# Performance work log

Hardware: AMD Instinct MI355X
Metric: run time of the kernel (lower is better)

The kernel has to match this reference:

```python
import jax, jax.numpy as jnp
import numpy as np
from jax import lax

B_SZ, SEQ, D_MODEL = 4, 1024, 1024
D_STATE, D_CONV, EXPAND = 16, 4, 2
D_INNER = EXPAND * D_MODEL
EPS = 1e-6


def layernorm(x, alpha, bias):
    # torch.std default is unbiased (ddof=1)
    mean = x.mean(axis=-1, keepdims=True)
    std = jnp.sqrt(jnp.var(x, axis=-1, keepdims=True, ddof=1))
    return alpha * (x - mean) / (std + EPS) + bias


def setup_inputs() -> dict:
    key = jax.random.key(0)
    ks = jax.random.split(key, 8)
    std = 0.02
    A = jnp.tile(jnp.arange(1, D_STATE + 1, dtype=jnp.float32)[None, :], (D_INNER, 1))
    return {
        "x": jax.random.normal(ks[0], (B_SZ, SEQ, D_MODEL), jnp.float32),
        "in_proj_w": jax.random.normal(ks[1], (2 * D_INNER, D_MODEL), jnp.float32) * std,
        "in_proj_b": jnp.zeros((2 * D_INNER,), jnp.float32),
        "conv_w": jax.random.normal(ks[2], (D_INNER, 1, D_CONV), jnp.float32) * std,
        "conv_b": jnp.zeros((D_INNER,), jnp.float32),
        "x_proj_w": jax.random.normal(ks[3], (2 * D_STATE, D_INNER), jnp.float32) * std,
        "x_proj_b": jnp.zeros((2 * D_STATE,), jnp.float32),
        "dt_proj_w": jax.random.normal(ks[4], (D_INNER, D_INNER), jnp.float32) * std,
        "dt_proj_b": jnp.zeros((D_INNER,), jnp.float32),
        "A_log": jnp.log(A),
        "D_param": jnp.ones((D_INNER,), jnp.float32),
        "out_proj_w": jax.random.normal(ks[5], (D_MODEL, D_INNER), jnp.float32) * std,
        "out_proj_b": jnp.zeros((D_MODEL,), jnp.float32),
        "norm_alpha": jnp.ones((D_MODEL,), jnp.float32),
        "norm_bias": jnp.zeros((D_MODEL,), jnp.float32),
        "in_norm_alpha": jnp.ones((D_MODEL,), jnp.float32),
        "in_norm_bias": jnp.zeros((D_MODEL,), jnp.float32),
    }


def selective_scan(x_conv, delta, A, Bm, Cm, D_param):
    # x_conv, delta: (B, L, E); A: (E, N); Bm, Cm: (B, L, N)
    L = x_conv.shape[1]

    def step(h, inp):
        xt, dt, bt, ct, t = inp  # (B,E),(B,E),(B,N),(B,N),()
        dA = jnp.exp(jnp.clip(dt[..., None] * A, -10.0, 0.0))          # (B,E,N)
        dBx = dt[..., None] * bt[:, None, :] * xt[..., None]           # (B,E,N)
        h = dA * h + dBx
        # periodic renormalization every 16 steps
        hn = jnp.clip(jnp.linalg.norm(h, axis=-1, keepdims=True), 1e-6, None)
        scale = jnp.where(hn > 10.0, 10.0 / hn, jnp.ones_like(hn))
        h = jnp.where(t % 16 == 15, h * scale, h)
        y = jnp.einsum('bn,ben->be', ct, h) + D_param * xt
        return h, y

    h0 = jnp.zeros((x_conv.shape[0], x_conv.shape[2], A.shape[1]), x_conv.dtype)
    xs = (x_conv.swapaxes(0, 1), delta.swapaxes(0, 1),
          Bm.swapaxes(0, 1), Cm.swapaxes(0, 1), jnp.arange(L))
    _, ys = lax.scan(step, h0, xs)
    return ys.swapaxes(0, 1)  # (B, L, E)


def reference(x, in_proj_w, in_proj_b, conv_w, conv_b, x_proj_w, x_proj_b,
              dt_proj_w, dt_proj_b, A_log, D_param, out_proj_w, out_proj_b,
              norm_alpha, norm_bias, in_norm_alpha, in_norm_bias):
    residual = x
    xn = layernorm(x, in_norm_alpha, in_norm_bias)
    xz = xn @ in_proj_w.T + in_proj_b                  # (B, L, 2E)
    x_in, z = jnp.split(xz, 2, axis=-1)
    # causal depthwise conv: pad left d_conv-1, no right pad == torch pad + truncate
    xc = lax.conv_general_dilated(
        x_in.swapaxes(1, 2), conv_w, window_strides=(1,),
        padding=[(D_CONV - 1, 0)], feature_group_count=D_INNER,
        dimension_numbers=('NCH', 'OIH', 'NCH')) + conv_b[None, :, None]
    x_conv = jax.nn.silu(xc.swapaxes(1, 2))            # (B, L, E)
    bc = x_conv @ x_proj_w.T + x_proj_b                # (B, L, 2N)
    Bm, Cm = jnp.split(bc, 2, axis=-1)
    delta = jax.nn.softplus(x_conv @ dt_proj_w.T + dt_proj_b)
    delta = jnp.clip(delta, 1e-4, 10.0)
    A = -jnp.exp(A_log)
    y = selective_scan(x_conv, delta, A, Bm, Cm, D_param)
    y = y * jax.nn.silu(z)
    out = y @ out_proj_w.T + out_proj_b
    # dropout is identity in eval mode
    return layernorm(residual + out, norm_alpha, norm_bias)
```

## Files before the change

### kernel.cpp

```cpp
#include <hip/hip_runtime.h>
#include <hip/hip_bf16.h>
#include <hip/hip_fp16.h>

#define B_SZ   4
#define SEQ    1024
#define DMODEL 1024
#define DSTATE 16
#define DINNER 2048
#define NROWS  (B_SZ * SEQ)
#define NCHUNK 64
#define NCHAIN (B_SZ * DINNER)
#define NDTXP  2176

typedef __attribute__((ext_vector_type(8))) _Float16 half8;
typedef __attribute__((ext_vector_type(4))) float f32x4;

__device__ __forceinline__ void gload_lds16(const void* g, void* l) {
  __builtin_amdgcn_global_load_lds(
      (const __attribute__((address_space(1))) unsigned int*)g,
      (__attribute__((address_space(3))) unsigned int*)l, 16, 0, 0);
}

__global__ __launch_bounds__(256) void f2h_pad(const float* __restrict__ src,
                                               _Float16* __restrict__ dst,
                                               int n_src, int n_dst) {
  int i = blockIdx.x * 256 + threadIdx.x;
  if (i < n_src) dst[i] = (_Float16)src[i];
  else if (i < n_dst) dst[i] = (_Float16)0.f;
}

__global__ __launch_bounds__(256) void concat_dtxp_w(const float* __restrict__ dt_w,
                                                     const float* __restrict__ xp_w,
                                                     _Float16* __restrict__ w) {
  int i = blockIdx.x * 256 + threadIdx.x;
  if (i >= NDTXP * DINNER) return;
  int row = i >> 11;
  float v = 0.f;
  if (row < 2048) v = dt_w[i];
  else if (row < 2080) v = xp_w[i - 2048 * DINNER];
  w[i] = (_Float16)v;
}
__global__ __launch_bounds__(256) void concat_dtxp_b(const float* __restrict__ dt_b,
                                                     const float* __restrict__ xp_b,
                                                     float* __restrict__ bias) {
  int i = blockIdx.x * 256 + threadIdx.x;
  if (i >= NDTXP) return;
  float v = 0.f;
  if (i < 2048) v = dt_b[i];
  else if (i < 2080) v = xp_b[i - 2048];
  bias[i] = v;
}

__global__ __launch_bounds__(256) void ln_kernel(
    const float* __restrict__ x, const float* __restrict__ alpha,
    const float* __restrict__ beta, _Float16* __restrict__ out_h) {
  int row = blockIdx.x, tid = threadIdx.x;
  float4 v = ((const float4*)(x + (size_t)row * DMODEL))[tid];
  float s  = v.x + v.y + v.z + v.w;
  float ss = v.x * v.x + v.y * v.y + v.z * v.z + v.w * v.w;
#pragma unroll
  for (int off = 1; off < 64; off <<= 1) {
    s += __shfl_xor(s, off);
    ss += __shfl_xor(ss, off);
  }
  __shared__ float red[8];
  int wid = tid >> 6, lane = tid & 63;
  if (lane == 0) { red[wid] = s; red[4 + wid] = ss; }
  __syncthreads();
  s = red[0] + red[1] + red[2] + red[3];
  ss = red[4] + red[5] + red[6] + red[7];
  float mean = s * (1.f / DMODEL);
  float var = (ss - (float)DMODEL * mean * mean) * (1.f / (DMODEL - 1));
  float inv = 1.f / (sqrtf(fmaxf(var, 0.f)) + 1e-6f);
  float4 al = ((const float4*)alpha)[tid];
  float4 be = ((const float4*)beta)[tid];
  _Float16* o = out_h + (size_t)row * DMODEL + tid * 4;
  o[0] = (_Float16)(al.x * (v.x - mean) * inv + be.x);
  o[1] = (_Float16)(al.y * (v.y - mean) * inv + be.y);
  o[2] = (_Float16)(al.z * (v.z - mean) * inv + be.z);
  o[3] = (_Float16)(al.w * (v.w - mean) * inv + be.w);
}

__global__ __launch_bounds__(256) void ln2_kernel(
    const float* __restrict__ x, const float* __restrict__ part,
    const float* __restrict__ alpha, const float* __restrict__ beta,
    float* __restrict__ out_f) {
  int row = blockIdx.x, tid = threadIdx.x;
  float4 v = ((const float4*)(x + (size_t)row * DMODEL))[tid];
  float4 a = ((const float4*)(part + (size_t)row * DMODEL))[tid];
  float4 b = ((const float4*)(part + (size_t)NROWS * DMODEL + (size_t)row * DMODEL))[tid];
  v.x += a.x + b.x; v.y += a.y + b.y; v.z += a.z + b.z; v.w += a.w + b.w;
  float s  = v.x + v.y + v.z + v.w;
  float ss = v.x * v.x + v.y * v.y + v.z * v.z + v.w * v.w;
#pragma unroll
  for (int off = 1; off < 64; off <<= 1) {
    s += __shfl_xor(s, off);
    ss += __shfl_xor(ss, off);
  }
  __shared__ float red[8];
  int wid = tid >> 6, lane = tid & 63;
  if (lane == 0) { red[wid] = s; red[4 + wid] = ss; }
  __syncthreads();
  s = red[0] + red[1] + red[2] + red[3];
  ss = red[4] + red[5] + red[6] + red[7];
  float mean = s * (1.f / DMODEL);
  float var = (ss - (float)DMODEL * mean * mean) * (1.f / (DMODEL - 1));
  float inv = 1.f / (sqrtf(fmaxf(var, 0.f)) + 1e-6f);
  float4 al = ((const float4*)alpha)[tid];
  float4 be = ((const float4*)beta)[tid];
  float4 r;
  r.x = al.x * (v.x - mean) * inv + be.x;
  r.y = al.y * (v.y - mean) * inv + be.y;
  r.z = al.z * (v.z - mean) * inv + be.z;
  r.w = al.w * (v.w - mean) * inv + be.w;
  ((float4*)(out_f + (size_t)row * DMODEL))[tid] = r;
}

template <int EPI, int BN>
__global__ __launch_bounds__(256, 4) void gemm_bt(
    const _Float16* __restrict__ A, const _Float16* __restrict__ B,
    const float* __restrict__ bias,
    void* __restrict__ Co, void* __restrict__ Co2,
    int lda, int ldb, int K, int ldc) {
  __shared__ __align__(16) _Float16 As[128 * 64];
  __shared__ __align__(16) _Float16 Bs[BN * 64];
  constexpr int NF = BN / 32;
  const int tid = threadIdx.x;
  const int nwgx = gridDim.x;
  const int nwg = nwgx * gridDim.y;
  const int orig = blockIdx.y * nwgx + blockIdx.x;
  const int cpx = nwg >> 3;
  const int id = (orig & 7) * cpx + (orig >> 3);
  const int m0 = (id / nwgx) * 128, n0 = (id % nwgx) * BN;
  const size_t koff = (size_t)blockIdx.z * K;

  const int lane = tid & 63;
  const int wid = tid >> 6;
  const int wr = wid >> 1, wc = wid & 1;
  const int r16 = lane & 15, q = lane >> 4;

  const int srow = tid >> 3, sslot = tid & 7;

  int aoff[2][4], boff[2][NF];
#pragma unroll
  for (int kk = 0; kk < 2; ++kk) {
#pragma unroll
    for (int mi = 0; mi < 4; ++mi) {
      int r = wr * 64 + mi * 16 + r16;
      aoff[kk][mi] = r * 128 + ((((kk << 2) + q) ^ (r & 7)) << 4);
    }
#pragma unroll
    for (int ni = 0; ni < NF; ++ni) {
      int r = wc * (BN / 2) + ni * 16 + r16;
      boff[kk][ni] = r * 128 + ((((kk << 2) + q) ^ (r & 7)) << 4);
    }
  }

  f32x4 acc[4][NF] = {};
  for (int k0 = 0; k0 < K; k0 += 64) {
    __syncthreads();
#pragma unroll
    for (int p = 0; p < 4; ++p) {
      int row = p * 32 + srow;
      int gs = sslot ^ (row & 7);
      gload_lds16(A + (size_t)(m0 + row) * lda + koff + k0 + gs * 8,
                  (char*)As + (p * 256 + tid) * 16);
    }
#pragma unroll
    for (int p = 0; p < BN / 32; ++p) {
      int row = p * 32 + srow;
      int gs = sslot ^ (row & 7);
      gload_lds16(B + (size_t)(n0 + row) * ldb + koff + k0 + gs * 8,
                  (char*)Bs + (p * 256 + tid) * 16);
    }
    __syncthreads();
#pragma unroll
    for (int kk = 0; kk < 2; ++kk) {
      half8 af[4], bf[NF];
#pragma unroll
      for (int mi = 0; mi < 4; ++mi) af[mi] = *(const half8*)((const char*)As + aoff[kk][mi]);
#pragma unroll
      for (int ni = 0; ni < NF; ++ni) bf[ni] = *(const half8*)((const char*)Bs + boff[kk][ni]);
#pragma unroll
      for (int mi = 0; mi < 4; ++mi)
#pragma unroll
        for (int ni = 0; ni < NF; ++ni)
          acc[mi][ni] =
              __builtin_amdgcn_mfma_f32_16x16x32_f16(af[mi], bf[ni], acc[mi][ni], 0, 0, 0);
    }
  }

#pragma unroll
  for (int mi = 0; mi < 4; ++mi) {
    int row = m0 + wr * 64 + mi * 16 + q * 4;
#pragma unroll
    for (int ni = 0; ni < NF; ++ni) {
      int col = n0 + wc * (BN / 2) + ni * 16 + r16;
      float bs = (blockIdx.z == 0) ? bias[col] : 0.f;
#pragma unroll
      for (int rr = 0; rr < 4; ++rr) {
        float v = acc[mi][ni][rr] + bs;
        if (EPI == 0) {
          ((_Float16*)Co)[(size_t)(row + rr) * ldc + col] = (_Float16)v;
        } else if (EPI == 2) {
          ((float*)Co)[(size_t)blockIdx.z * NROWS * ldc +
                       (size_t)(row + rr) * ldc + col] = v;
        } else {
          if (col < 2048) {
            float sp = v > 15.f ? v : log1pf(__expf(v));
            ((_Float16*)Co)[(size_t)(row + rr) * 2048 + col] =
                (_Float16)fminf(10.f, fmaxf(1e-4f, sp));
          } else {
            ((float*)Co2)[(size_t)(row + rr) * 128 + (col - 2048)] = v;
          }
        }
      }
    }
  }
}

__global__ __launch_bounds__(256) void conv_silu(const _Float16* __restrict__ xz,
                                                 const float* __restrict__ w,
                                                 const float* __restrict__ cb,
                                                 _Float16* __restrict__ xc) {
  int idx = blockIdx.x * 256 + threadIdx.x;
  int e = idx & (DINNER - 1);
  int t = (idx >> 11) & (SEQ - 1);
  int b = idx >> 21;
  const _Float16* base = xz + (size_t)b * SEQ * (2 * DINNER) + e;
  float acc = cb[e];
  float4 wv = *(const float4*)(w + e * 4);
  const float* wp = (const float*)&wv;
#pragma unroll
  for (int j = 0; j < 4; ++j) {
    int tt = t - 3 + j;
    if (tt >= 0) acc += wp[j] * (float)base[(size_t)tt * (2 * DINNER)];
  }
  float r = acc / (1.f + __expf(-acc));
  xc[idx] = (_Float16)r;
}

__global__ __launch_bounds__(256) void scan_p1(
    const _Float16* __restrict__ xc, const _Float16* __restrict__ dth,
    const float* __restrict__ bcp, const float* __restrict__ A_log,
    _Float16* __restrict__ Pout, _Float16* __restrict__ Qout) {
  int tid = threadIdx.x;
  int bx = blockIdx.x;
  int c = bx >> 5;
  int b = (bx >> 3) & 3;
  int e = ((bx & 7) << 8) + tid;
  float A[16];
  {
    const float4* ap = (const float4*)(A_log + (size_t)e * DSTATE);
#pragma unroll
    for (int i = 0; i < 4; ++i) {
      float4 v = ap[i];
      A[4 * i + 0] = -__expf(v.x); A[4 * i + 1] = -__expf(v.y);
      A[4 * i + 2] = -__expf(v.z); A[4 * i + 3] = -__expf(v.w);
    }
  }
  size_t row0 = (size_t)b * SEQ + (size_t)c * 16;
  const _Float16* pdt = dth + row0 * DINNER + e;
  const _Float16* px  = xc  + row0 * DINNER + e;
  const float*    pb  = bcp + row0 * 128;
  float P[16], q[16];
#pragma unroll
  for (int n = 0; n < 16; ++n) { P[n] = 1.f; q[n] = 0.f; }
  for (int u = 0; u < 16; ++u) {
    float dtv = (float)pdt[(size_t)u * DINNER];
    float xv  = (float)px[(size_t)u * DINNER];
    float dtx = dtv * xv;
    const float4* Bp = (const float4*)(pb + (size_t)u * 128);
    float Bv[16];
#pragma unroll
    for (int i = 0; i < 4; ++i) {
      float4 t4 = Bp[i];
      Bv[4 * i + 0] = t4.x; Bv[4 * i + 1] = t4.y;
      Bv[4 * i + 2] = t4.z; Bv[4 * i + 3] = t4.w;
    }
#pragma unroll
    for (int n = 0; n < 16; ++n) {
      float da = __expf(fmaxf(dtv * A[n], -10.f));
      P[n] *= da;
      q[n] = da * q[n] + dtx * Bv[n];
    }
  }
  size_t chain = (size_t)b * DINNER + e;
  size_t base = ((size_t)c * NCHAIN + chain) * 16;
  half8 p0, p1, q0, q1;
#pragma unroll
  for (int n = 0; n < 8; ++n) {
    p0[n] = (_Float16)P[n]; p1[n] = (_Float16)P[n + 8];
    q0[n] = (_Float16)q[n]; q1[n] = (_Float16)q[n + 8];
  }
  ((half8*)(Pout + base))[0] = p0; ((half8*)(Pout + base))[1] = p1;
  ((half8*)(Qout + base))[0] = q0; ((half8*)(Qout + base))[1] = q1;
}

__global__ __launch_bounds__(256) void scan_p2(
    _Float16* __restrict__ Pbuf, const _Float16* __restrict__ Qbuf) {
  int chain = blockIdx.x * 256 + threadIdx.x;
  float h[16];
#pragma unroll
  for (int n = 0; n < 16; ++n) h[n] = 0.f;
  for (int c = 0; c < NCHUNK; ++c) {
    size_t base = ((size_t)c * NCHAIN + chain) * 16;
    half8 p0 = ((const half8*)(Pbuf + base))[0];
    half8 p1 = ((const half8*)(Pbuf + base))[1];
    half8 q0 = ((const half8*)(Qbuf + base))[0];
    half8 q1 = ((const half8*)(Qbuf + base))[1];
    float hold[16];
#pragma unroll
    for (int n = 0; n < 16; ++n) hold[n] = h[n];
#pragma unroll
    for (int n = 0; n < 8; ++n) {
      h[n]     = (float)p0[n] * h[n]     + (float)q0[n];
      h[n + 8] = (float)p1[n] * h[n + 8] + (float)q1[n];
    }
    float hn2 = 0.f;
#pragma unroll
    for (int n = 0; n < 16; ++n) hn2 += h[n] * h[n];
    float hn = fmaxf(sqrtf(hn2), 1e-6f);
    if (hn > 10.f) {
      float sc = 10.f / hn;
#pragma unroll
      for (int n = 0; n < 16; ++n) h[n] *= sc;
    }
    if (c > 0) {
      size_t pb2 = ((size_t)(c - 1) * NCHAIN + chain) * 16;
      half8 s0, s1;
#pragma unroll
      for (int n = 0; n < 8; ++n) {
        s0[n] = (_Float16)hold[n]; s1[n] = (_Float16)hold[n + 8];
      }
      ((half8*)(Pbuf + pb2))[0] = s0;
      ((half8*)(Pbuf + pb2))[1] = s1;
    }
  }
}

__global__ __launch_bounds__(256) void scan_p3(
    const _Float16* __restrict__ xc, const _Float16* __restrict__ dth,
    const float* __restrict__ bcp, const _Float16* __restrict__ xz,
    const float* __restrict__ A_log, const float* __restrict__ Dp,
    const _Float16* __restrict__ Hbuf, _Float16* __restrict__ y) {
  int tid = threadIdx.x;
  int bx = blockIdx.x;
  int c = bx >> 5;
  int b = (bx >> 3) & 3;
  int e = ((bx & 7) << 8) + tid;
  float A[16];
  {
    const float4* ap = (const float4*)(A_log + (size_t)e * DSTATE);
#pragma unroll
    for (int i = 0; i < 4; ++i) {
      float4 v = ap[i];
      A[4 * i + 0] = -__expf(v.x); A[4 * i + 1] = -__expf(v.y);
      A[4 * i + 2] = -__expf(v.z); A[4 * i + 3] = -__expf(v.w);
    }
  }
  float Dv = Dp[e];
  size_t chain = (size_t)b * DINNER + e;
  float h[16];
  if (c == 0) {
#pragma unroll
    for (int n = 0; n < 16; ++n) h[n] = 0.f;
  } else {
    size_t hbase = ((size_t)(c - 1) * NCHAIN + chain) * 16;
    half8 h0 = ((const half8*)(Hbuf + hbase))[0];
    half8 h1 = ((const half8*)(Hbuf + hbase))[1];
#pragma unroll
    for (int n = 0; n < 8; ++n) { h[n] = (float)h0[n]; h[n + 8] = (float)h1[n]; }
  }
  size_t row0 = (size_t)b * SEQ + (size_t)c * 16;
  const _Float16* pdt = dth + row0 * DINNER + e;
  const _Float16* px  = xc  + row0 * DINNER + e;
  const _Float16* pz  = xz + row0 * (2 * DINNER) + DINNER + e;
  const float*    pb  = bcp + row0 * 128;
  _Float16*      yout = y + row0 * DINNER + e;
  for (int u = 0; u < 16; ++u) {
    float dtv = (float)pdt[(size_t)u * DINNER];
    float xv  = (float)px[(size_t)u * DINNER];
    float zv  = (float)pz[(size_t)u * (2 * DINNER)];
    float dtx = dtv * xv;
    const float4* Bp = (const float4*)(pb + (size_t)u * 128);
    float Bv[16], Cv[16];
#pragma unroll
    for (int i = 0; i < 4; ++i) {
      float4 t4 = Bp[i];
      Bv[4 * i + 0] = t4.x; Bv[4 * i + 1] = t4.y;
      Bv[4 * i + 2] = t4.z; Bv[4 * i + 3] = t4.w;
      float4 c4 = Bp[i + 4];
      Cv[4 * i + 0] = c4.x; Cv[4 * i + 1] = c4.y;
      Cv[4 * i + 2] = c4.z; Cv[4 * i + 3] = c4.w;
    }
#pragma unroll
    for (int n = 0; n < 16; ++n) {
      float da = __expf(fmaxf(dtv * A[n], -10.f));
      h[n] = da * h[n] + dtx * Bv[n];
    }
    if (u == 15) {
      float hn2 = 0.f;
#pragma unroll
      for (int n = 0; n < 16; ++n) hn2 += h[n] * h[n];
      float hn = fmaxf(sqrtf(hn2), 1e-6f);
      if (hn > 10.f) {
        float sc = 10.f / hn;
#pragma unroll
        for (int n = 0; n < 16; ++n) h[n] *= sc;
      }
    }
    float s0 = 0.f, s1 = 0.f, s2 = 0.f, s3 = 0.f;
#pragma unroll
    for (int n = 0; n < 4; ++n) {
      s0 += Cv[n] * h[n];
      s1 += Cv[n + 4] * h[n + 4];
      s2 += Cv[n + 8] * h[n + 8];
      s3 += Cv[n + 12] * h[n + 12];
    }
    float p = (s0 + s1) + (s2 + s3);
    float yv = p + Dv * xv;
    float sig = zv / (1.f + __expf(-zv));
    yout[(size_t)u * DINNER] = (_Float16)(yv * sig);
  }
}

extern "C" void kernel_launch(void* const* d_in, const int* in_sizes, int n_in,
                              void* d_out, int out_size, void* d_ws, size_t ws_size,
                              hipStream_t stream) {
  const float* x      = (const float*)d_in[0];
  const float* in_w   = (const float*)d_in[1];
  const float* in_b   = (const float*)d_in[2];
  const float* conv_w = (const float*)d_in[3];
  const float* conv_b = (const float*)d_in[4];
  const float* xp_w   = (const float*)d_in[5];
  const float* xp_b   = (const float*)d_in[6];
  const float* dt_w   = (const float*)d_in[7];
  const float* dt_b   = (const float*)d_in[8];
  const float* A_log  = (const float*)d_in[9];
  const float* Dp     = (const float*)d_in[10];
  const float* out_w  = (const float*)d_in[11];
  const float* out_b  = (const float*)d_in[12];
  const float* nal    = (const float*)d_in[13];
  const float* nbi    = (const float*)d_in[14];
  const float* inal   = (const float*)d_in[15];
  const float* inbi   = (const float*)d_in[16];

  char* ws = (char*)d_ws;
  size_t o = 0;
  auto alloc = [&](size_t bytes) {
    void* p = ws + o;
    o += (bytes + 255) & ~(size_t)255;
    return p;
  };
  _Float16* w_in_h  = (_Float16*)alloc((size_t)(2 * DINNER) * DMODEL * 2);
  _Float16* w_dtxp  = (_Float16*)alloc((size_t)NDTXP * DINNER * 2);
  float*    b_dtxp  = (float*)alloc((size_t)NDTXP * 4);
  _Float16* w_out_h = (_Float16*)alloc((size_t)DMODEL * DINNER * 2);
  _Float16* xn_h    = (_Float16*)alloc((size_t)NROWS * DMODEL * 2);
  _Float16* xz_h    = (_Float16*)alloc((size_t)NROWS * (2 * DINNER) * 2);
  _Float16* xc_h    = (_Float16*)alloc((size_t)NROWS * DINNER * 2);
  _Float16* dt_h    = (_Float16*)alloc((size_t)NROWS * DINNER * 2);
  float*    bcp     = (float*)alloc((size_t)NROWS * 128 * 4);
  _Float16* y_h     = (_Float16*)alloc((size_t)NROWS * DINNER * 2);
  _Float16* Pbuf    = (_Float16*)alloc((size_t)NCHUNK * NCHAIN * 16 * 2);
  float*    part    = (float*)xz_h;
  _Float16* Qbuf    = w_in_h;

  (void)in_sizes; (void)n_in; (void)out_size; (void)ws_size;

  f2h_pad<<<(2 * DINNER * DMODEL + 255) / 256, 256, 0, stream>>>(in_w, w_in_h,
      2 * DINNER * DMODEL, 2 * DINNER * DMODEL);
  concat_dtxp_w<<<(NDTXP * DINNER + 255) / 256, 256, 0, stream>>>(dt_w, xp_w, w_dtxp);
  concat_dtxp_b<<<(NDTXP + 255) / 256, 256, 0, stream>>>(dt_b, xp_b, b_dtxp);
  f2h_pad<<<(DMODEL * DINNER + 255) / 256, 256, 0, stream>>>(out_w, w_out_h,
      DMODEL * DINNER, DMODEL * DINNER);

  ln_kernel<<<NROWS, 256, 0, stream>>>(x, inal, inbi, xn_h);

  gemm_bt<0, 128><<<dim3(32, 32), 256, 0, stream>>>(
      xn_h, w_in_h, in_b, xz_h, nullptr, DMODEL, DMODEL, DMODEL, 2 * DINNER);

  conv_silu<<<(NROWS * DINNER) / 256, 256, 0, stream>>>(xz_h, conv_w, conv_b, xc_h);

  gemm_bt<3, 64><<<dim3(34, 32), 256, 0, stream>>>(
      xc_h, w_dtxp, b_dtxp, dt_h, bcp, DINNER, DINNER, DINNER, 0);

  scan_p1<<<2048, 256, 0, stream>>>(xc_h, dt_h, bcp, A_log, Pbuf, Qbuf);
  scan_p2<<<NCHAIN / 256, 256, 0, stream>>>(Pbuf, Qbuf);
  scan_p3<<<2048, 256, 0, stream>>>(xc_h, dt_h, bcp, xz_h, A_log, Dp, Pbuf, y_h);

  gemm_bt<2, 64><<<dim3(16, 32, 2), 256, 0, stream>>>(
      y_h, w_out_h, out_b, part, nullptr, DINNER, DINNER, DINNER / 2, DMODEL);

  ln2_kernel<<<NROWS, 256, 0, stream>>>(x, part, nal, nbi, (float*)d_out);
}
```

Baseline: 352.3 us.

## Split-K dt/xproj and out_proj GEMMs with fp16 partials, fold softplus into scans

```diff
diff --git a/kernel.cpp b/kernel.cpp
--- a/kernel.cpp
+++ b/kernel.cpp
@@ -13,6 +13,7 @@
 #define NDTXP  2176
 
 typedef __attribute__((ext_vector_type(8))) _Float16 half8;
+typedef __attribute__((ext_vector_type(4))) _Float16 half4;
 typedef __attribute__((ext_vector_type(4))) float f32x4;
 
 __device__ __forceinline__ void gload_lds16(const void* g, void* l) {
@@ -82,14 +83,17 @@
 }
 
 __global__ __launch_bounds__(256) void ln2_kernel(
-    const float* __restrict__ x, const float* __restrict__ part,
+    const float* __restrict__ x, const _Float16* __restrict__ part,
     const float* __restrict__ alpha, const float* __restrict__ beta,
     float* __restrict__ out_f) {
   int row = blockIdx.x, tid = threadIdx.x;
   float4 v = ((const float4*)(x + (size_t)row * DMODEL))[tid];
-  float4 a = ((const float4*)(part + (size_t)row * DMODEL))[tid];
-  float4 b = ((const float4*)(part + (size_t)NROWS * DMODEL + (size_t)row * DMODEL))[tid];
-  v.x += a.x + b.x; v.y += a.y + b.y; v.z += a.z + b.z; v.w += a.w + b.w;
+#pragma unroll
+  for (int sl = 0; sl < 4; ++sl) {
+    half4 p = *(const half4*)(part + (size_t)sl * NROWS * DMODEL +
+                              (size_t)row * DMODEL + tid * 4);
+    v.x += (float)p[0]; v.y += (float)p[1]; v.z += (float)p[2]; v.w += (float)p[3];
+  }
   float s  = v.x + v.y + v.z + v.w;
   float ss = v.x * v.x + v.y * v.y + v.z * v.z + v.w * v.w;
 #pragma unroll
@@ -190,6 +194,9 @@
     }
   }
 
+  _Float16* Cout;
+  if (EPI == 0) Cout = (_Float16*)Co + (size_t)blockIdx.z * NROWS * ldc;
+  else          Cout = blockIdx.z ? (_Float16*)Co2 : (_Float16*)Co;
 #pragma unroll
   for (int mi = 0; mi < 4; ++mi) {
     int row = m0 + wr * 64 + mi * 16 + q * 4;
@@ -200,20 +207,7 @@
 #pragma unroll
       for (int rr = 0; rr < 4; ++rr) {
         float v = acc[mi][ni][rr] + bs;
-        if (EPI == 0) {
-          ((_Float16*)Co)[(size_t)(row + rr) * ldc + col] = (_Float16)v;
-        } else if (EPI == 2) {
-          ((float*)Co)[(size_t)blockIdx.z * NROWS * ldc +
-                       (size_t)(row + rr) * ldc + col] = v;
-        } else {
-          if (col < 2048) {
-            float sp = v > 15.f ? v : log1pf(__expf(v));
-            ((_Float16*)Co)[(size_t)(row + rr) * 2048 + col] =
-                (_Float16)fminf(10.f, fmaxf(1e-4f, sp));
-          } else {
-            ((float*)Co2)[(size_t)(row + rr) * 128 + (col - 2048)] = v;
-          }
-        }
+        Cout[(size_t)(row + rr) * ldc + col] = (_Float16)v;
       }
     }
   }
@@ -240,9 +234,15 @@
   xc[idx] = (_Float16)r;
 }
 
+__device__ __forceinline__ float dt_from_raw(float r0, float r1) {
+  float dr = r0 + r1;
+  float sp = dr > 15.f ? dr : log1pf(__expf(dr));
+  return fminf(10.f, fmaxf(1e-4f, sp));
+}
+
 __global__ __launch_bounds__(256) void scan_p1(
-    const _Float16* __restrict__ xc, const _Float16* __restrict__ dth,
-    const float* __restrict__ bcp, const float* __restrict__ A_log,
+    const _Float16* __restrict__ xc, const _Float16* __restrict__ dtr0,
+    const _Float16* __restrict__ dtr1, const float* __restrict__ A_log,
     _Float16* __restrict__ Pout, _Float16* __restrict__ Qout) {
   int tid = threadIdx.x;
   int bx = blockIdx.x;
@@ -260,23 +260,27 @@
     }
   }
   size_t row0 = (size_t)b * SEQ + (size_t)c * 16;
-  const _Float16* pdt = dth + row0 * DINNER + e;
-  const _Float16* px  = xc  + row0 * DINNER + e;
-  const float*    pb  = bcp + row0 * 128;
+  const _Float16* px  = xc + row0 * DINNER + e;
+  const _Float16* pd0 = dtr0 + row0 * NDTXP + e;
+  const _Float16* pd1 = dtr1 + row0 * NDTXP + e;
+  const _Float16* pb0 = dtr0 + row0 * NDTXP + 2048;
+  const _Float16* pb1 = dtr1 + row0 * NDTXP + 2048;
   float P[16], q[16];
 #pragma unroll
   for (int n = 0; n < 16; ++n) { P[n] = 1.f; q[n] = 0.f; }
   for (int u = 0; u < 16; ++u) {
-    float dtv = (float)pdt[(size_t)u * DINNER];
+    float dtv = dt_from_raw((float)pd0[(size_t)u * NDTXP], (float)pd1[(size_t)u * NDTXP]);
     float xv  = (float)px[(size_t)u * DINNER];
     float dtx = dtv * xv;
-    const float4* Bp = (const float4*)(pb + (size_t)u * 128);
+    half8 b0 = ((const half8*)(pb0 + (size_t)u * NDTXP))[0];
+    half8 b0h = ((const half8*)(pb0 + (size_t)u * NDTXP))[1];
+    half8 b1 = ((const half8*)(pb1 + (size_t)u * NDTXP))[0];
+    half8 b1h = ((const half8*)(pb1 + (size_t)u * NDTXP))[1];
     float Bv[16];
 #pragma unroll
-    for (int i = 0; i < 4; ++i) {
-      float4 t4 = Bp[i];
-      Bv[4 * i + 0] = t4.x; Bv[4 * i + 1] = t4.y;
-      Bv[4 * i + 2] = t4.z; Bv[4 * i + 3] = t4.w;
+    for (int n = 0; n < 8; ++n) {
+      Bv[n] = (float)b0[n] + (float)b1[n];
+      Bv[n + 8] = (float)b0h[n] + (float)b1h[n];
     }
 #pragma unroll
     for (int n = 0; n < 16; ++n) {
@@ -340,8 +344,8 @@
 }
 
 __global__ __launch_bounds__(256) void scan_p3(
-    const _Float16* __restrict__ xc, const _Float16* __restrict__ dth,
-    const float* __restrict__ bcp, const _Float16* __restrict__ xz,
+    const _Float16* __restrict__ xc, const _Float16* __restrict__ dtr0,
+    const _Float16* __restrict__ dtr1, const _Float16* __restrict__ xz,
     const float* __restrict__ A_log, const float* __restrict__ Dp,
     const _Float16* __restrict__ Hbuf, _Float16* __restrict__ y) {
   int tid = threadIdx.x;
@@ -373,26 +377,33 @@
     for (int n = 0; n < 8; ++n) { h[n] = (float)h0[n]; h[n + 8] = (float)h1[n]; }
   }
   size_t row0 = (size_t)b * SEQ + (size_t)c * 16;
-  const _Float16* pdt = dth + row0 * DINNER + e;
-  const _Float16* px  = xc  + row0 * DINNER + e;
+  const _Float16* px  = xc + row0 * DINNER + e;
+  const _Float16* pd0 = dtr0 + row0 * NDTXP + e;
+  const _Float16* pd1 = dtr1 + row0 * NDTXP + e;
+  const _Float16* pb0 = dtr0 + row0 * NDTXP + 2048;
+  const _Float16* pb1 = dtr1 + row0 * NDTXP + 2048;
   const _Float16* pz  = xz + row0 * (2 * DINNER) + DINNER + e;
-  const float*    pb  = bcp + row0 * 128;
   _Float16*      yout = y + row0 * DINNER + e;
   for (int u = 0; u < 16; ++u) {
-    float dtv = (float)pdt[(size_t)u * DINNER];
+    float dtv = dt_from_raw((float)pd0[(size_t)u * NDTXP], (float)pd1[(size_t)u * NDTXP]);
     float xv  = (float)px[(size_t)u * DINNER];
     float zv  = (float)pz[(size_t)u * (2 * DINNER)];
     float dtx = dtv * xv;
-    const float4* Bp = (const float4*)(pb + (size_t)u * 128);
+    half8 b0 = ((const half8*)(pb0 + (size_t)u * NDTXP))[0];
+    half8 b0h = ((const half8*)(pb0 + (size_t)u * NDTXP))[1];
+    half8 c0 = ((const half8*)(pb0 + (size_t)u * NDTXP))[2];
+    half8 c0h = ((const half8*)(pb0 + (size_t)u * NDTXP))[3];
+    half8 b1 = ((const half8*)(pb1 + (size_t)u * NDTXP))[0];
+    half8 b1h = ((const half8*)(pb1 + (size_t)u * NDTXP))[1];
+    half8 c1 = ((const half8*)(pb1 + (size_t)u * NDTXP))[2];
+    half8 c1h = ((const half8*)(pb1 + (size_t)u * NDTXP))[3];
     float Bv[16], Cv[16];
 #pragma unroll
-    for (int i = 0; i < 4; ++i) {
-      float4 t4 = Bp[i];
-      Bv[4 * i + 0] = t4.x; Bv[4 * i + 1] = t4.y;
-      Bv[4 * i + 2] = t4.z; Bv[4 * i + 3] = t4.w;
-      float4 c4 = Bp[i + 4];
-      Cv[4 * i + 0] = c4.x; Cv[4 * i + 1] = c4.y;
-      Cv[4 * i + 2] = c4.z; Cv[4 * i + 3] = c4.w;
+    for (int n = 0; n < 8; ++n) {
+      Bv[n] = (float)b0[n] + (float)b1[n];
+      Bv[n + 8] = (float)b0h[n] + (float)b1h[n];
+      Cv[n] = (float)c0[n] + (float)c1[n];
+      Cv[n + 8] = (float)c0h[n] + (float)c1h[n];
     }
 #pragma unroll
     for (int n = 0; n < 16; ++n) {
@@ -454,18 +465,19 @@
     return p;
   };
   _Float16* w_in_h  = (_Float16*)alloc((size_t)(2 * DINNER) * DMODEL * 2);
+  _Float16* xn_h    = (_Float16*)alloc((size_t)NROWS * DMODEL * 2);
+  alloc((size_t)1 << 20);
   _Float16* w_dtxp  = (_Float16*)alloc((size_t)NDTXP * DINNER * 2);
   float*    b_dtxp  = (float*)alloc((size_t)NDTXP * 4);
   _Float16* w_out_h = (_Float16*)alloc((size_t)DMODEL * DINNER * 2);
-  _Float16* xn_h    = (_Float16*)alloc((size_t)NROWS * DMODEL * 2);
   _Float16* xz_h    = (_Float16*)alloc((size_t)NROWS * (2 * DINNER) * 2);
   _Float16* xc_h    = (_Float16*)alloc((size_t)NROWS * DINNER * 2);
-  _Float16* dt_h    = (_Float16*)alloc((size_t)NROWS * DINNER * 2);
-  float*    bcp     = (float*)alloc((size_t)NROWS * 128 * 4);
   _Float16* y_h     = (_Float16*)alloc((size_t)NROWS * DINNER * 2);
   _Float16* Pbuf    = (_Float16*)alloc((size_t)NCHUNK * NCHAIN * 16 * 2);
-  float*    part    = (float*)xz_h;
-  _Float16* Qbuf    = w_in_h;
+  _Float16* dtr1    = (_Float16*)alloc((size_t)NROWS * NDTXP * 2);
+  _Float16* Qbuf    = (_Float16*)alloc((size_t)NCHUNK * NCHAIN * 16 * 2);
+  _Float16* dtr0    = w_in_h;
+  _Float16* part    = xz_h;
 
   (void)in_sizes; (void)n_in; (void)out_size; (void)ws_size;
 
@@ -483,15 +495,15 @@
 
   conv_silu<<<(NROWS * DINNER) / 256, 256, 0, stream>>>(xz_h, conv_w, conv_b, xc_h);
 
-  gemm_bt<3, 64><<<dim3(34, 32), 256, 0, stream>>>(
-      xc_h, w_dtxp, b_dtxp, dt_h, bcp, DINNER, DINNER, DINNER, 0);
-
-  scan_p1<<<2048, 256, 0, stream>>>(xc_h, dt_h, bcp, A_log, Pbuf, Qbuf);
+  gemm_bt<5, 128><<<dim3(17, 32, 2), 256, 0, stream>>>(
+      xc_h, w_dtxp, b_dtxp, dtr0, dtr1, DINNER, DINNER, DINNER / 2, NDTXP);
+
+  scan_p1<<<2048, 256, 0, stream>>>(xc_h, dtr0, dtr1, A_log, Pbuf, Qbuf);
   scan_p2<<<NCHAIN / 256, 256, 0, stream>>>(Pbuf, Qbuf);
-  scan_p3<<<2048, 256, 0, stream>>>(xc_h, dt_h, bcp, xz_h, A_log, Dp, Pbuf, y_h);
-
-  gemm_bt<2, 64><<<dim3(16, 32, 2), 256, 0, stream>>>(
-      y_h, w_out_h, out_b, part, nullptr, DINNER, DINNER, DINNER / 2, DMODEL);
+  scan_p3<<<2048, 256, 0, stream>>>(xc_h, dtr0, dtr1, xz_h, A_log, Dp, Pbuf, y_h);
+
+  gemm_bt<0, 128><<<dim3(8, 32, 4), 256, 0, stream>>>(
+      y_h, w_out_h, out_b, part, nullptr, DINNER, DINNER, DINNER / 4, DMODEL);
 
   ln2_kernel<<<NROWS, 256, 0, stream>>>(x, part, nal, nbi, (float*)d_out);
 }
```

Result: slower. 412.6 us (+17.1%).
